# Performance work log

Hardware: AMD Instinct MI355X
Metric: run time of the kernel (lower is better)

## Reference

```python
import jax, jax.numpy as jnp
import numpy as np

B, N, D, H = 4, 2048, 256, 4
DH = D // H
EPS = 1e-5


def setup_inputs() -> dict:
    key = jax.random.key(0)
    ks = jax.random.split(key, 12)
    s = 0.02
    return {
        "x0": jax.random.normal(ks[0], (B, N, D), jnp.float32),
        "x1": jax.random.normal(ks[1], (B, N, D), jnp.float32),
        "w_qk": jax.random.normal(ks[2], (D, D), jnp.float32) * s,
        "b_qk": jax.random.normal(ks[3], (D,), jnp.float32) * s,
        "w_v": jax.random.normal(ks[4], (D, D), jnp.float32) * s,
        "b_v": jax.random.normal(ks[5], (D,), jnp.float32) * s,
        "w_out": jax.random.normal(ks[6], (D, D), jnp.float32) * s,
        "b_out": jax.random.normal(ks[7], (D,), jnp.float32) * s,
        "w_f1": jax.random.normal(ks[8], (2 * D, 2 * D), jnp.float32) * s,
        "b_f1": jax.random.normal(ks[9], (2 * D,), jnp.float32) * s,
        "ln_g": jnp.ones((2 * D,), jnp.float32),
        "ln_b": jnp.zeros((2 * D,), jnp.float32),
        "w_f2": jax.random.normal(ks[10], (2 * D, D), jnp.float32) * s,
        "b_f2": jax.random.normal(ks[11], (D,), jnp.float32) * s,
    }


def _split_heads(t):  # [b, n, h*d] -> [b, h, n, d]
    b, n, _ = t.shape
    return t.reshape(b, n, H, DH).transpose(0, 2, 1, 3)


def _merge_heads(t):  # [b, h, n, d] -> [b, n, h*d]
    b, h, n, d = t.shape
    return t.transpose(0, 2, 1, 3).reshape(b, n, h * d)


def _layernorm(x, g, b):
    mu = jnp.mean(x, axis=-1, keepdims=True)
    var = jnp.mean(jnp.square(x - mu), axis=-1, keepdims=True)
    return (x - mu) * jax.lax.rsqrt(var + EPS) * g + b


def reference(x0, x1, w_qk, b_qk, w_v, b_v, w_out, b_out,
              w_f1, b_f1, ln_g, ln_b, w_f2, b_f2):
    scale = DH ** -0.5
    qk0 = _split_heads(x0 @ w_qk + b_qk) * scale ** 0.5
    qk1 = _split_heads(x1 @ w_qk + b_qk) * scale ** 0.5
    v0 = _split_heads(x0 @ w_v + b_v)
    v1 = _split_heads(x1 @ w_v + b_v)

    # shared similarity matrix, bisoftmax: row-softmax for 0->1, col-softmax for 1->0
    sim = jnp.einsum('bhid,bhjd->bhij', qk0, qk1)  # [b,h,n0,n1]
    a0 = jax.nn.softmax(sim, axis=-1)              # over n1
    a1 = jax.nn.softmax(sim, axis=-2)              # over n0
    m0 = jnp.einsum('bhij,bhjd->bhid', a0, v1)     # [b,h,n0,d]
    m1 = jnp.einsum('bhji,bhjd->bhid', a1, v0)     # [b,h,n1,d]

    m0 = _merge_heads(m0) @ w_out + b_out
    m1 = _merge_heads(m1) @ w_out + b_out

    def ffn(x, m):
        h = jnp.concatenate([x, m], axis=-1) @ w_f1 + b_f1
        h = jax.nn.gelu(_layernorm(h, ln_g, ln_b), approximate=False)
        return x + h @ w_f2 + b_f2

    return ffn(x0, m0), ffn(x1, m1)
```

## Files before the change

### kernel.cpp

```cpp
#include <hip/hip_runtime.h>
#include <cstdint>
#include <cstddef>


#define QKS2 0.4246609001440095f

typedef short bf16x8 __attribute__((ext_vector_type(8)));
typedef float f32x4  __attribute__((ext_vector_type(4)));

__device__ __forceinline__ uint16_t f2bf(float f){
  union { float f; uint32_t u; } v; v.f = f;
  uint32_t r = v.u + 0x7FFFu + ((v.u >> 16) & 1u);
  return (uint16_t)(r >> 16);
}
__device__ __forceinline__ uint16_t f2bf_trunc(float f){
  union { float f; uint32_t u; } v; v.f = f;
  return (uint16_t)(v.u >> 16);
}
__device__ __forceinline__ float bf2f(uint16_t h){
  union { uint32_t u; float f; } v; v.u = ((uint32_t)h) << 16; return v.f;
}

__device__ __forceinline__ void gl_lds16(const void* g, void* l){
  void* g2 = const_cast<void*>(g);
  __builtin_amdgcn_global_load_lds((__attribute__((address_space(1))) void*)g2,
                                   (__attribute__((address_space(3))) void*)l,
                                   16, 0, 0);
}

__global__ __launch_bounds__(256) void conv_x_k(const float* __restrict__ x0,
                                                const float* __restrict__ x1,
                                                uint16_t* __restrict__ xb){
  const float* src = blockIdx.z ? x1 : x0;
  uint16_t* dst = xb + (size_t)blockIdx.z * 2097152;
  size_t i = ((size_t)blockIdx.x * 256 + threadIdx.x) * 4;
  float4 v = *(const float4*)(src + i);
  uint2 o;
  o.x = (uint32_t)f2bf(v.x) | ((uint32_t)f2bf(v.y) << 16);
  o.y = (uint32_t)f2bf(v.z) | ((uint32_t)f2bf(v.w) << 16);
  *(uint2*)(dst + i) = o;
}

__global__ __launch_bounds__(256) void conv_w_k(
    const float* w0, const float* w1, const float* w2, const float* w3, const float* w4,
    uint16_t* t0, uint16_t* t1, uint16_t* t2, uint16_t* t3, uint16_t* t4){
  const int z = blockIdx.z;
  const float* src = z==0? w0 : z==1? w1 : z==2? w2 : z==3? w3 : w4;
  uint16_t*   dst  = z==0? t0 : z==1? t1 : z==2? t2 : z==3? t3 : t4;
  const int K = (z>=3)? 512 : 256;
  const int N = (z==3)? 512 : 256;
  int idx = blockIdx.x * 256 + threadIdx.x;
  if (idx >= (K*N)/4) return;
  int k = idx / (N/4);
  int n = (idx % (N/4)) * 4;
  float4 v = *(const float4*)(src + (size_t)k*N + n);
  dst[(size_t)(n+0)*K + k] = f2bf(v.x);
  dst[(size_t)(n+1)*K + k] = f2bf(v.y);
  dst[(size_t)(n+2)*K + k] = f2bf(v.z);
  dst[(size_t)(n+3)*K + k] = f2bf(v.w);
}

struct GemmArgs {
  const uint16_t* A0; const uint16_t* A1;
  const uint16_t* A2_0; const uint16_t* A2_1;
  const uint16_t* Wt0; const uint16_t* Wt1;
  const float* bias0; const float* bias1;
  uint16_t* out0; uint16_t* out1; uint16_t* out2; uint16_t* out3;
  float* fout; const float* xf0; const float* xf1;
  int K;
};

template<int MODE>
__global__ __launch_bounds__(256, 4) void gemm_k(GemmArgs a){
  __shared__ __align__(16) uint16_t As[64*64];
  __shared__ __align__(16) uint16_t Bs[128*64];
  const int tid = threadIdx.x;
  const int w = tid >> 6, l = tid & 63;
  const int z = blockIdx.z;
  const int which = (MODE==0) ? (z & 1) : z;
  const int wsel  = (MODE==0) ? (z >> 1) : 0;
  const int K = a.K;
  const int m0 = blockIdx.x * 64;
  const int n0 = blockIdx.y * 128;
  const uint16_t* Wt   = wsel ? a.Wt1 : a.Wt0;
  const float* bias    = wsel ? a.bias1 : a.bias0;
  const uint16_t* Ab   = which ? a.A1 : a.A0;
  const uint16_t* Ab2  = which ? a.A2_1 : a.A2_0;

  f32x4 acc[4][2];
  #pragma unroll
  for (int i=0;i<4;++i)
    #pragma unroll
    for (int j=0;j<2;++j) acc[i][j] = (f32x4){0.f,0.f,0.f,0.f};

  const int lrow8 = l >> 3, lch = l & 7;
  const int swch = (lch ^ lrow8) * 8;
  const int quad = l >> 4, l15 = l & 15, h7 = l15 & 7;

  for (int k0 = 0; k0 < K; k0 += 64){
    __syncthreads();
    const uint16_t* Asrc; int lda;
    if (MODE == 2){
      Asrc = (k0 < 256) ? (Ab + k0) : (Ab2 + (k0 - 256));
      lda = 256;
    } else { Asrc = Ab + k0; lda = K; }
    #pragma unroll
    for (int j=0;j<2;++j){
      int wi = w*2 + j;
      int row = wi*8 + lrow8;
      gl_lds16(Asrc + (size_t)(m0 + row)*lda + swch, &As[wi*512]);
    }
    #pragma unroll
    for (int j=0;j<4;++j){
      int wi = w*4 + j;
      int row = wi*8 + lrow8;
      gl_lds16(Wt + (size_t)(n0 + row)*K + k0 + swch, &Bs[wi*512]);
    }
    __syncthreads();
    #pragma unroll
    for (int kc=0;kc<2;++kc){
      const int fch = ((kc*4 + quad) ^ h7) * 8;
      bf16x8 af[4], bfr[2];
      #pragma unroll
      for (int rt=0;rt<4;++rt)
        af[rt] = *(const bf16x8*)&As[(rt*16 + l15)*64 + fch];
      #pragma unroll
      for (int ct=0;ct<2;++ct)
        bfr[ct] = *(const bf16x8*)&Bs[(w*32 + ct*16 + l15)*64 + fch];
      #pragma unroll
      for (int rt=0;rt<4;++rt)
        #pragma unroll
        for (int ct=0;ct<2;++ct)
          acc[rt][ct] = __builtin_amdgcn_mfma_f32_16x16x32_bf16(af[rt], bfr[ct], acc[rt][ct], 0,0,0);
    }
  }

  #pragma unroll
  for (int rt=0;rt<4;++rt){
    const int r0 = m0 + rt*16 + (quad<<2);
    #pragma unroll
    for (int ct=0;ct<2;++ct){
      const int c = n0 + w*32 + ct*16 + l15;
      const float bv = bias[c];
      if (MODE == 0){
        if (wsel == 0){
          uint16_t* q = which ? a.out1 : a.out0;
          #pragma unroll
          for (int i=0;i<4;++i)
            q[(size_t)(r0+i)*256 + c] = f2bf((acc[rt][ct][i] + bv) * QKS2);
        } else {
          uint16_t* vt = which ? a.out3 : a.out2;
          const int bb = r0 >> 11, nn = r0 & 2047;
          const int hh = c >> 6,  dd = c & 63;
          uint2 pk;
          pk.x = (uint32_t)f2bf(acc[rt][ct][0] + bv) | ((uint32_t)f2bf(acc[rt][ct][1] + bv) << 16);
          pk.y = (uint32_t)f2bf(acc[rt][ct][2] + bv) | ((uint32_t)f2bf(acc[rt][ct][3] + bv) << 16);
          *(uint2*)(vt + ((size_t)((bb*4 + hh)*64 + dd))*2048 + nn) = pk;
        }
      } else if (MODE == 1){
        uint16_t* o = which ? a.out1 : a.out0;
        #pragma unroll
        for (int i=0;i<4;++i)
          o[(size_t)(r0+i)*256 + c] = f2bf(acc[rt][ct][i] + bv);
      } else if (MODE == 2){
        uint16_t* o = which ? a.out1 : a.out0;
        #pragma unroll
        for (int i=0;i<4;++i)
          o[(size_t)(r0+i)*512 + c] = f2bf(acc[rt][ct][i] + bv);
      } else {
        const float* xf = which ? a.xf1 : a.xf0;
        float* fo = a.fout + (size_t)which * 2097152;
        #pragma unroll
        for (int i=0;i<4;++i)
          fo[(size_t)(r0+i)*256 + c] = acc[rt][ct][i] + bv + xf[(size_t)(r0+i)*256 + c];
      }
    }
  }
}

#define PSTRIDE 76

__global__ __launch_bounds__(256, 4) void flash_k(
    const uint16_t* __restrict__ qk0, const uint16_t* __restrict__ qk1,
    const uint16_t* __restrict__ vt0, const uint16_t* __restrict__ vt1,
    uint16_t* __restrict__ m0b, uint16_t* __restrict__ m1b){
  __shared__ __align__(16) uint16_t Qs[64*64];
  __shared__ __align__(16) uint16_t Ks[64*64];
  __shared__ __align__(16) uint16_t Vs[64*64];
  __shared__ __align__(16) uint16_t Ps[64*PSTRIDE];
  const int tid = threadIdx.x;
  const int w = tid >> 6, l = tid & 63;
  const int qt = blockIdx.x;
  const int bh = blockIdx.y;
  const int dir = blockIdx.z;
  const int b = bh >> 2, h = bh & 3;
  const uint16_t* Q   = dir ? qk1 : qk0;
  const uint16_t* Kg  = dir ? qk0 : qk1;
  const uint16_t* Vt  = dir ? vt0 : vt1;
  uint16_t* outp      = dir ? m1b : m0b;

  const int qrow0 = b*2048 + qt*64;
  const int lrow8 = l >> 3, lch = l & 7;
  const int swch = (lch ^ lrow8) * 8;
  const int quad = l >> 4, l15 = l & 15, h7 = l15 & 7;

  const short ONE = (short)0x3F80;
  const bf16x8 ones = {ONE,ONE,ONE,ONE,ONE,ONE,ONE,ONE};

  #pragma unroll
  for (int j=0;j<2;++j){
    int wi = w*2 + j;
    int row = wi*8 + lrow8;
    gl_lds16(Q + (size_t)(qrow0 + row)*256 + h*64 + swch, &Qs[wi*512]);
  }
  __syncthreads();
  bf16x8 qf[2];
  #pragma unroll
  for (int kc=0;kc<2;++kc)
    qf[kc] = *(const bf16x8*)&Qs[(w*16 + l15)*64 + (((kc*4 + quad) ^ h7)*8)];

  f32x4 o[4];
  f32x4 lacc = (f32x4){0.f,0.f,0.f,0.f};
  #pragma unroll
  for (int dt=0;dt<4;++dt) o[dt] = (f32x4){0.f,0.f,0.f,0.f};

  const size_t vbase = (size_t)bh * 64 * 2048;

  for (int kt=0; kt<32; ++kt){
    __syncthreads();
    #pragma unroll
    for (int j=0;j<2;++j){
      int wi = w*2 + j;
      int row = wi*8 + lrow8;
      gl_lds16(Kg + (size_t)(b*2048 + kt*64 + row)*256 + h*64 + swch, &Ks[wi*512]);
      gl_lds16(Vt + vbase + (size_t)row*2048 + kt*64 + swch, &Vs[wi*512]);
    }
    __syncthreads();

    bf16x8 kf[4][2];
    #pragma unroll
    for (int ct=0;ct<4;++ct)
      #pragma unroll
      for (int kc=0;kc<2;++kc)
        kf[ct][kc] = *(const bf16x8*)&Ks[(ct*16 + l15)*64 + (((kc*4 + quad) ^ h7)*8)];
    f32x4 s[4];
    #pragma unroll
    for (int ct=0;ct<4;++ct){
      f32x4 z4 = (f32x4){0.f,0.f,0.f,0.f};
      z4 = __builtin_amdgcn_mfma_f32_16x16x32_bf16(qf[0], kf[ct][0], z4, 0,0,0);
      s[ct] = __builtin_amdgcn_mfma_f32_16x16x32_bf16(qf[1], kf[ct][1], z4, 0,0,0);
    }

    #pragma unroll
    for (int reg=0;reg<4;++reg){
      const int prow = (w*16 + quad*4 + reg) * PSTRIDE;
      #pragma unroll
      for (int ct=0;ct<4;++ct){
        float p = __builtin_amdgcn_exp2f(s[ct][reg]);
        Ps[prow + ct*16 + l15] = f2bf_trunc(p);
      }
    }

    bf16x8 vf[4][2], pf[2];
    #pragma unroll
    for (int dt=0;dt<4;++dt)
      #pragma unroll
      for (int kc=0;kc<2;++kc)
        vf[dt][kc] = *(const bf16x8*)&Vs[(dt*16 + l15)*64 + (((kc*4 + quad) ^ h7)*8)];
    #pragma unroll
    for (int kc=0;kc<2;++kc)
      pf[kc] = *(const bf16x8*)&Ps[(w*16 + l15)*PSTRIDE + kc*32 + quad*8];
    lacc = __builtin_amdgcn_mfma_f32_16x16x32_bf16(pf[0], ones, lacc, 0,0,0);
    lacc = __builtin_amdgcn_mfma_f32_16x16x32_bf16(pf[1], ones, lacc, 0,0,0);
    #pragma unroll
    for (int dt=0;dt<4;++dt){
      o[dt] = __builtin_amdgcn_mfma_f32_16x16x32_bf16(pf[0], vf[dt][0], o[dt], 0,0,0);
      o[dt] = __builtin_amdgcn_mfma_f32_16x16x32_bf16(pf[1], vf[dt][1], o[dt], 0,0,0);
    }
  }

  float inv[4];
  #pragma unroll
  for (int reg=0;reg<4;++reg) inv[reg] = 1.0f / lacc[reg];
  const int r0 = qrow0 + w*16 + quad*4;
  #pragma unroll
  for (int dt=0;dt<4;++dt){
    const int col = h*64 + dt*16 + l15;
    #pragma unroll
    for (int reg=0;reg<4;++reg)
      outp[(size_t)(r0+reg)*256 + col] = f2bf(o[dt][reg] * inv[reg]);
  }
}

__global__ __launch_bounds__(256) void lngelu_k(const uint16_t* __restrict__ hpre,
                                                const float* __restrict__ g,
                                                const float* __restrict__ bb,
                                                uint16_t* __restrict__ h){
  const int row = blockIdx.x*4 + (threadIdx.x >> 6);
  const int l = threadIdx.x & 63;
  const uint16_t* rp = hpre + (size_t)row*512 + l*8;
  uint4 raw = *(const uint4*)rp;
  uint32_t wv[4] = {raw.x, raw.y, raw.z, raw.w};
  float x[8];
  #pragma unroll
  for (int j=0;j<4;++j){
    x[2*j]   = bf2f((uint16_t)(wv[j] & 0xFFFFu));
    x[2*j+1] = bf2f((uint16_t)(wv[j] >> 16));
  }
  float s = 0.f;
  #pragma unroll
  for (int j=0;j<8;++j) s += x[j];
  #pragma unroll
  for (int off=1; off<64; off<<=1) s += __shfl_xor(s, off, 64);
  float mu = s * (1.0f/512.0f);
  float vs = 0.f;
  #pragma unroll
  for (int j=0;j<8;++j){ float d = x[j]-mu; vs += d*d; }
  #pragma unroll
  for (int off=1; off<64; off<<=1) vs += __shfl_xor(vs, off, 64);
  float rstd = rsqrtf(vs*(1.0f/512.0f) + 1e-5f);
  const float* gp = g + l*8;
  const float* bp = bb + l*8;
  uint32_t ow[4];
  #pragma unroll
  for (int j=0;j<4;++j){
    float y0 = (x[2*j]-mu)*rstd*gp[2*j] + bp[2*j];
    float y1 = (x[2*j+1]-mu)*rstd*gp[2*j+1] + bp[2*j+1];
    float g0 = 0.5f*y0*(1.0f + erff(y0*0.70710678118f));
    float g1 = 0.5f*y1*(1.0f + erff(y1*0.70710678118f));
    ow[j] = (uint32_t)f2bf(g0) | ((uint32_t)f2bf(g1) << 16);
  }
  uint4 out4 = {ow[0], ow[1], ow[2], ow[3]};
  *(uint4*)(h + (size_t)row*512 + l*8) = out4;
}

extern "C" void kernel_launch(void* const* d_in, const int* in_sizes, int n_in,
                              void* d_out, int out_size, void* d_ws, size_t ws_size,
                              hipStream_t stream){
  (void)in_sizes; (void)n_in; (void)out_size; (void)ws_size;
  const float* x0   = (const float*)d_in[0];
  const float* x1   = (const float*)d_in[1];
  const float* w_qk = (const float*)d_in[2];
  const float* b_qk = (const float*)d_in[3];
  const float* w_v  = (const float*)d_in[4];
  const float* b_v  = (const float*)d_in[5];
  const float* w_out= (const float*)d_in[6];
  const float* b_out= (const float*)d_in[7];
  const float* w_f1 = (const float*)d_in[8];
  const float* b_f1 = (const float*)d_in[9];
  const float* ln_g = (const float*)d_in[10];
  const float* ln_b = (const float*)d_in[11];
  const float* w_f2 = (const float*)d_in[12];
  const float* b_f2 = (const float*)d_in[13];

  char* ws = (char*)d_ws;
  uint16_t* xb    = (uint16_t*)(ws);
  uint16_t* wqkT  = (uint16_t*)(ws +  8388608);
  uint16_t* wvT   = (uint16_t*)(ws +  8519680);
  uint16_t* woutT = (uint16_t*)(ws +  8650752);
  uint16_t* wf1T  = (uint16_t*)(ws +  8781824);
  uint16_t* wf2T  = (uint16_t*)(ws +  9306112);
  uint16_t* qk0b  = (uint16_t*)(ws +  9568256);
  uint16_t* qk1b  = (uint16_t*)(ws + 13762560);
  uint16_t* vt0b  = (uint16_t*)(ws + 17956864);
  uint16_t* vt1b  = (uint16_t*)(ws + 22151168);
  uint16_t* m0b   = (uint16_t*)(ws + 26345472);
  uint16_t* m1b   = (uint16_t*)(ws + 30539776);
  uint16_t* mp0b  = (uint16_t*)(ws + 34734080);
  uint16_t* mp1b  = (uint16_t*)(ws + 38928384);
  uint16_t* hpreb = qk0b;
  uint16_t* hb    = m0b;

  conv_x_k<<<dim3(2048,1,2), 256, 0, stream>>>(x0, x1, xb);
  conv_w_k<<<dim3(256,1,5), 256, 0, stream>>>(w_qk, w_v, w_out, w_f1, w_f2,
                                              wqkT, wvT, woutT, wf1T, wf2T);

  GemmArgs g0 = {};
  g0.A0 = xb; g0.A1 = xb + 2097152;
  g0.Wt0 = wqkT; g0.Wt1 = wvT;
  g0.bias0 = b_qk; g0.bias1 = b_v;
  g0.out0 = qk0b; g0.out1 = qk1b; g0.out2 = vt0b; g0.out3 = vt1b;
  g0.K = 256;
  gemm_k<0><<<dim3(128,2,4), 256, 0, stream>>>(g0);

  flash_k<<<dim3(32,16,2), 256, 0, stream>>>(qk0b, qk1b, vt0b, vt1b, m0b, m1b);

  GemmArgs g1 = {};
  g1.A0 = m0b; g1.A1 = m1b;
  g1.Wt0 = woutT; g1.bias0 = b_out;
  g1.out0 = mp0b; g1.out1 = mp1b;
  g1.K = 256;
  gemm_k<1><<<dim3(128,2,2), 256, 0, stream>>>(g1);

  GemmArgs g2 = {};
  g2.A0 = xb; g2.A1 = xb + 2097152;
  g2.A2_0 = mp0b; g2.A2_1 = mp1b;
  g2.Wt0 = wf1T; g2.bias0 = b_f1;
  g2.out0 = hpreb; g2.out1 = hpreb + 4194304;
  g2.K = 512;
  gemm_k<2><<<dim3(128,4,2), 256, 0, stream>>>(g2);

  lngelu_k<<<dim3(4096,1,1), 256, 0, stream>>>(hpreb, ln_g, ln_b, hb);

  GemmArgs g3 = {};
  g3.A0 = hb; g3.A1 = hb + 4194304;
  g3.Wt0 = wf2T; g3.bias0 = b_f2;
  g3.fout = (float*)d_out;
  g3.xf0 = x0; g3.xf1 = x1;
  g3.K = 512;
  gemm_k<3><<<dim3(128,2,2), 256, 0, stream>>>(g3);
}
```

Measured before the change: 221.7 us.

## Switch flash attention to 32x32x16 MFMA with two-wave blocks

Measured after the change: 221.8 us. No clear change (+0.1%).

```diff
diff --git a/kernel.cpp b/kernel.cpp
--- a/kernel.cpp
+++ b/kernel.cpp
@@ -7,6 +7,7 @@
 
 typedef short bf16x8 __attribute__((ext_vector_type(8)));
 typedef float f32x4  __attribute__((ext_vector_type(4)));
+typedef float f32x16 __attribute__((ext_vector_type(16)));
 
 __device__ __forceinline__ uint16_t f2bf(float f){
   union { float f; uint32_t u; } v; v.f = f;
@@ -178,16 +179,13 @@
   }
 }
 
-#define PSTRIDE 76
-
-__global__ __launch_bounds__(256, 4) void flash_k(
+__global__ __launch_bounds__(128, 2) void flash_k(
     const uint16_t* __restrict__ qk0, const uint16_t* __restrict__ qk1,
     const uint16_t* __restrict__ vt0, const uint16_t* __restrict__ vt1,
     uint16_t* __restrict__ m0b, uint16_t* __restrict__ m1b){
-  __shared__ __align__(16) uint16_t Qs[64*64];
   __shared__ __align__(16) uint16_t Ks[64*64];
   __shared__ __align__(16) uint16_t Vs[64*64];
-  __shared__ __align__(16) uint16_t Ps[64*PSTRIDE];
+  __shared__ __align__(16) uint16_t Ps[64*64];
   const int tid = threadIdx.x;
   const int w = tid >> 6, l = tid & 63;
   const int qt = blockIdx.x;
@@ -201,94 +199,102 @@
 
   const int qrow0 = b*2048 + qt*64;
   const int lrow8 = l >> 3, lch = l & 7;
-  const int swch = (lch ^ lrow8) * 8;
-  const int quad = l >> 4, l15 = l & 15, h7 = l15 & 7;
+  const int l31 = l & 31, lhi = l >> 5;
+  const int rsub = l31 >> 3;
 
   const short ONE = (short)0x3F80;
   const bf16x8 ones = {ONE,ONE,ONE,ONE,ONE,ONE,ONE,ONE};
 
   #pragma unroll
-  for (int j=0;j<2;++j){
-    int wi = w*2 + j;
-    int row = wi*8 + lrow8;
-    gl_lds16(Q + (size_t)(qrow0 + row)*256 + h*64 + swch, &Qs[wi*512]);
+  for (int j=0;j<4;++j){
+    int g = w*4 + j;
+    int row = g*8 + lrow8;
+    int sc = (lch ^ lrow8 ^ (g & 7)) * 8;
+    gl_lds16(Q + (size_t)(qrow0 + row)*256 + h*64 + sc, &Ps[g*512]);
   }
   __syncthreads();
-  bf16x8 qf[2];
-  #pragma unroll
-  for (int kc=0;kc<2;++kc)
-    qf[kc] = *(const bf16x8*)&Qs[(w*16 + l15)*64 + (((kc*4 + quad) ^ h7)*8)];
-
-  f32x4 o[4];
-  f32x4 lacc = (f32x4){0.f,0.f,0.f,0.f};
-  #pragma unroll
-  for (int dt=0;dt<4;++dt) o[dt] = (f32x4){0.f,0.f,0.f,0.f};
+  bf16x8 qf[4];
+  {
+    const int qmask = (l & 7) ^ ((w*4 + rsub) & 7);
+    #pragma unroll
+    for (int ks=0;ks<4;++ks){
+      int ch = (ks*2 + lhi) ^ qmask;
+      qf[ks] = *(const bf16x8*)&Ps[(w*32 + l31)*64 + ch*8];
+    }
+  }
+
+  f32x16 o0, o1, lacc;
+  #pragma unroll
+  for (int i=0;i<16;++i){ o0[i]=0.f; o1[i]=0.f; lacc[i]=0.f; }
 
   const size_t vbase = (size_t)bh * 64 * 2048;
+  const int pmask = (l & 7) ^ ((w*4 + rsub) & 7);
 
   for (int kt=0; kt<32; ++kt){
     __syncthreads();
     #pragma unroll
-    for (int j=0;j<2;++j){
-      int wi = w*2 + j;
-      int row = wi*8 + lrow8;
-      gl_lds16(Kg + (size_t)(b*2048 + kt*64 + row)*256 + h*64 + swch, &Ks[wi*512]);
-      gl_lds16(Vt + vbase + (size_t)row*2048 + kt*64 + swch, &Vs[wi*512]);
+    for (int j=0;j<4;++j){
+      int g = w*4 + j;
+      int row = g*8 + lrow8;
+      int sc = (lch ^ lrow8 ^ (g & 7)) * 8;
+      gl_lds16(Kg + (size_t)(b*2048 + kt*64 + row)*256 + h*64 + sc, &Ks[g*512]);
+      gl_lds16(Vt + vbase + (size_t)row*2048 + kt*64 + sc, &Vs[g*512]);
     }
     __syncthreads();
 
-    bf16x8 kf[4][2];
-    #pragma unroll
-    for (int ct=0;ct<4;++ct)
-      #pragma unroll
-      for (int kc=0;kc<2;++kc)
-        kf[ct][kc] = *(const bf16x8*)&Ks[(ct*16 + l15)*64 + (((kc*4 + quad) ^ h7)*8)];
-    f32x4 s[4];
-    #pragma unroll
-    for (int ct=0;ct<4;++ct){
-      f32x4 z4 = (f32x4){0.f,0.f,0.f,0.f};
-      z4 = __builtin_amdgcn_mfma_f32_16x16x32_bf16(qf[0], kf[ct][0], z4, 0,0,0);
-      s[ct] = __builtin_amdgcn_mfma_f32_16x16x32_bf16(qf[1], kf[ct][1], z4, 0,0,0);
-    }
-
-    #pragma unroll
-    for (int reg=0;reg<4;++reg){
-      const int prow = (w*16 + quad*4 + reg) * PSTRIDE;
-      #pragma unroll
-      for (int ct=0;ct<4;++ct){
-        float p = __builtin_amdgcn_exp2f(s[ct][reg]);
-        Ps[prow + ct*16 + l15] = f2bf_trunc(p);
-      }
-    }
-
-    bf16x8 vf[4][2], pf[2];
-    #pragma unroll
-    for (int dt=0;dt<4;++dt)
-      #pragma unroll
-      for (int kc=0;kc<2;++kc)
-        vf[dt][kc] = *(const bf16x8*)&Vs[(dt*16 + l15)*64 + (((kc*4 + quad) ^ h7)*8)];
-    #pragma unroll
-    for (int kc=0;kc<2;++kc)
-      pf[kc] = *(const bf16x8*)&Ps[(w*16 + l15)*PSTRIDE + kc*32 + quad*8];
-    lacc = __builtin_amdgcn_mfma_f32_16x16x32_bf16(pf[0], ones, lacc, 0,0,0);
-    lacc = __builtin_amdgcn_mfma_f32_16x16x32_bf16(pf[1], ones, lacc, 0,0,0);
-    #pragma unroll
-    for (int dt=0;dt<4;++dt){
-      o[dt] = __builtin_amdgcn_mfma_f32_16x16x32_bf16(pf[0], vf[dt][0], o[dt], 0,0,0);
-      o[dt] = __builtin_amdgcn_mfma_f32_16x16x32_bf16(pf[1], vf[dt][1], o[dt], 0,0,0);
-    }
-  }
-
-  float inv[4];
-  #pragma unroll
-  for (int reg=0;reg<4;++reg) inv[reg] = 1.0f / lacc[reg];
-  const int r0 = qrow0 + w*16 + quad*4;
-  #pragma unroll
-  for (int dt=0;dt<4;++dt){
-    const int col = h*64 + dt*16 + l15;
-    #pragma unroll
-    for (int reg=0;reg<4;++reg)
-      outp[(size_t)(r0+reg)*256 + col] = f2bf(o[dt][reg] * inv[reg]);
+    f32x16 s0, s1;
+    #pragma unroll
+    for (int i=0;i<16;++i){ s0[i]=0.f; s1[i]=0.f; }
+    #pragma unroll
+    for (int ks=0;ks<4;++ks){
+      int ch0 = ((ks*2 + lhi) ^ (l & 7) ^ rsub) * 8;
+      int ch1 = ((ks*2 + lhi) ^ (l & 7) ^ (4 + rsub)) * 8;
+      bf16x8 k0 = *(const bf16x8*)&Ks[l31*64 + ch0];
+      bf16x8 k1 = *(const bf16x8*)&Ks[(32 + l31)*64 + ch1];
+      s0 = __builtin_amdgcn_mfma_f32_32x32x16_bf16(qf[ks], k0, s0, 0,0,0);
+      s1 = __builtin_amdgcn_mfma_f32_32x32x16_bf16(qf[ks], k1, s1, 0,0,0);
+    }
+
+    #pragma unroll
+    for (int reg=0; reg<16; ++reg){
+      int rm   = (reg&3) + 8*(reg>>2) + 4*lhi;
+      int row  = w*32 + rm;
+      int mask = ((rm & 7) ^ ((w*4 + (reg>>2)) & 7));
+      int kc0  = (l31 >> 3);
+      float p0 = __builtin_amdgcn_exp2f(s0[reg]);
+      Ps[row*64 + ((kc0 ^ mask))*8 + (l31 & 7)] = f2bf_trunc(p0);
+      float p1 = __builtin_amdgcn_exp2f(s1[reg]);
+      Ps[row*64 + (((4 + kc0) ^ mask))*8 + (l31 & 7)] = f2bf_trunc(p1);
+    }
+
+    bf16x8 pf[4];
+    #pragma unroll
+    for (int ks=0;ks<4;++ks){
+      int ch = ((ks*2 + lhi) ^ pmask) * 8;
+      pf[ks] = *(const bf16x8*)&Ps[(w*32 + l31)*64 + ch];
+    }
+    #pragma unroll
+    for (int ks=0;ks<4;++ks)
+      lacc = __builtin_amdgcn_mfma_f32_32x32x16_bf16(pf[ks], ones, lacc, 0,0,0);
+    #pragma unroll
+    for (int ks=0;ks<4;++ks){
+      int ch0 = ((ks*2 + lhi) ^ (l & 7) ^ rsub) * 8;
+      int ch1 = ((ks*2 + lhi) ^ (l & 7) ^ (4 + rsub)) * 8;
+      bf16x8 v0 = *(const bf16x8*)&Vs[l31*64 + ch0];
+      bf16x8 v1 = *(const bf16x8*)&Vs[(32 + l31)*64 + ch1];
+      o0 = __builtin_amdgcn_mfma_f32_32x32x16_bf16(pf[ks], v0, o0, 0,0,0);
+      o1 = __builtin_amdgcn_mfma_f32_32x32x16_bf16(pf[ks], v1, o1, 0,0,0);
+    }
+  }
+
+  const int c0 = h*64 + l31;
+  #pragma unroll
+  for (int reg=0; reg<16; ++reg){
+    float inv = 1.0f / lacc[reg];
+    int rm  = (reg&3) + 8*(reg>>2) + 4*lhi;
+    size_t row = (size_t)(qrow0 + w*32 + rm);
+    outp[row*256 + c0]      = f2bf(o0[reg] * inv);
+    outp[row*256 + c0 + 32] = f2bf(o1[reg] * inv);
   }
 }
 
@@ -383,7 +389,7 @@
   g0.K = 256;
   gemm_k<0><<<dim3(128,2,4), 256, 0, stream>>>(g0);
 
-  flash_k<<<dim3(32,16,2), 256, 0, stream>>>(qk0b, qk1b, vt0b, vt1b, m0b, m1b);
+  flash_k<<<dim3(32,16,2), 128, 0, stream>>>(qk0b, qk1b, vt0b, vt1b, m0b, m1b);
 
   GemmArgs g1 = {};
   g1.A0 = m0b; g1.A1 = m1b;
```
